# Optimization experiments

Hardware: AMD Instinct MI355X
Metric: run time of the kernel (lower is better)

The kernel has to match this reference:

```python
import jax, jax.numpy as jnp
import numpy as np

TOPK_RATIO = 0.1
THRESHOLD = 0.25
OUT_DIM = 256
STATS_DIM = 18
NEG = -1e30  # sentinel for invalid pixels when sorting (values are probs in [0,1])


def setup_inputs() -> dict:
    key = jax.random.key(0)
    k1, k2, k3, k4, k5, k6, k7 = jax.random.split(key, 7)
    B, C, H, W = 16, 4, 512, 512
    evidence_logits = jax.random.normal(k1, (B, C, H, W), dtype=jnp.float32)
    severity_map = jax.random.normal(k2, (B, 1, H, W), dtype=jnp.float32)
    target_mask = jax.random.uniform(k3, (B, 1, H, W), dtype=jnp.float32)
    # LayerNorm(18) params (torch defaults: weight=1, bias=0)
    ln_w = jnp.ones((STATS_DIM,), jnp.float32)
    ln_b = jnp.zeros((STATS_DIM,), jnp.float32)
    # Linear(18, out_dim) and Linear(out_dim, out_dim)
    w1 = jax.random.normal(k4, (STATS_DIM, OUT_DIM), dtype=jnp.float32) * 0.1
    b1 = jax.random.normal(k5, (OUT_DIM,), dtype=jnp.float32) * 0.01
    w2 = jax.random.normal(k6, (OUT_DIM, OUT_DIM), dtype=jnp.float32) * 0.05
    b2 = jax.random.normal(k7, (OUT_DIM,), dtype=jnp.float32) * 0.01
    return {"evidence_logits": evidence_logits, "severity_map": severity_map,
            "target_mask": target_mask, "ln_w": ln_w, "ln_b": ln_b,
            "w1": w1, "b1": b1, "w2": w2, "b2": b2}


def _forward(evidence_logits, severity_map, target_mask, ln_w, ln_b, w1, b1, w2, b2):
    B, C, H, W = evidence_logits.shape
    N = H * W
    prob = jax.nn.softmax(evidence_logits, axis=1).reshape(B, C, N).transpose(0, 2, 1)  # [B,N,4]
    sev = jax.nn.sigmoid(severity_map).reshape(B, N)                                    # [B,N]
    # mask is same spatial size as logits, so nearest resize is identity
    valid = target_mask.reshape(B, N) > 0.5                                             # [B,N] bool
    validf = valid.astype(prob.dtype)
    total = validf.sum(axis=-1)                                                         # [B]
    has = total > 0
    safe_total = jnp.maximum(total, 1.0)
    # k = max(1, round(total * ratio)); total>=1 implies k<=total
    k = jnp.maximum(1, jnp.round(total * TOPK_RATIO)).astype(jnp.int32)                 # [B]

    # per-class masked mean / max
    class_mean = jnp.einsum('bnc,bn->bc', prob, validf) / safe_total[:, None]           # [B,4]
    class_max = jnp.max(jnp.where(valid[:, :, None], prob, NEG), axis=1)                # [B,4]
    class_max = jnp.where(has[:, None], class_max, 0.0)

    # top-k means for 4 class channels + severity at once: sort desc, cumsum, gather at k-1
    vals = jnp.concatenate([prob, sev[:, :, None]], axis=-1)                            # [B,N,5]
    masked = jnp.where(valid[:, :, None], vals, NEG)
    sorted_desc = jnp.sort(masked, axis=1)[:, ::-1, :]                                  # [B,N,5]
    csum = jnp.cumsum(sorted_desc, axis=1)
    idx = (k - 1).astype(jnp.int32)[:, None, None]                                      # [B,1,1]
    topk_mean = jnp.take_along_axis(csum, jnp.broadcast_to(idx, (B, 1, 5)), axis=1)[:, 0, :]
    topk_mean = topk_mean / k[:, None].astype(prob.dtype)                               # [B,5]
    topk_mean = jnp.where(has[:, None], topk_mean, 0.0)
    class_topk = topk_mean[:, :4]                                                       # [B,4]
    sev_topk = topk_mean[:, 4:5]                                                        # [B,1]

    sev_mean = jnp.where(has, jnp.sum(sev * validf, axis=-1) / safe_total, 0.0)[:, None]
    sev_max = jnp.where(has, jnp.max(jnp.where(valid, sev, NEG), axis=-1), 0.0)[:, None]

    damaged_ind = (prob[:, :, 1] + prob[:, :, 2] + prob[:, :, 3] > THRESHOLD).astype(prob.dtype)
    high_ind = (prob[:, :, 2] + prob[:, :, 3] > THRESHOLD).astype(prob.dtype)
    damaged = jnp.where(has, jnp.sum(damaged_ind * validf, axis=-1) / safe_total, 0.0)   # [B]
    high = jnp.where(has, jnp.sum(high_ind * validf, axis=-1) / safe_total, 0.0)         # [B]
    tar = jnp.where(has, validf.mean(axis=-1), 0.0)                                      # [B]

    stats = jnp.concatenate([class_mean, class_max, class_topk,
                             sev_mean, sev_max, sev_topk,
                             damaged[:, None], high[:, None], tar[:, None]], axis=-1)    # [B,18]

    # LayerNorm(18), eps=1e-5
    mu = stats.mean(axis=-1, keepdims=True)
    var = jnp.mean((stats - mu) ** 2, axis=-1, keepdims=True)
    normed = (stats - mu) * jax.lax.rsqrt(var + 1e-5) * ln_w + ln_b
    h1 = jax.nn.gelu(normed @ w1 + b1, approximate=False)
    projected = h1 @ w2 + b2                                                             # [B,256]
    return stats, projected, damaged, high, tar


def reference(evidence_logits, severity_map, target_mask, ln_w, ln_b, w1, b1, w2, b2):
    return _forward(evidence_logits, severity_map, target_mask, ln_w, ln_b, w1, b1, w2, b2)
```

## Files before the change

### kernel.cpp

```cpp
#include <hip/hip_runtime.h>
#include <math.h>

#define NB 512
#define CHN 5

static constexpr int kN = 512 * 512;
static constexpr int kB = 16;
static constexpr int kChunks = 64;
static constexpr int kThreads1 = 512;
static constexpr int kPixPerBlock = kN / kChunks;
static constexpr int kF4PerBlock = kPixPerBlock / 4;
static constexpr int kGroups = kF4PerBlock / kThreads1;
static constexpr int kHist = CHN * NB;

static constexpr size_t GHIST_OFF = 0;
static constexpr size_t SPART_OFF = GHIST_OFF + (size_t)kB * kHist * 4;
static constexpr size_t PART_OFF  = SPART_OFF + (size_t)kB * kChunks * 16 * 4;
static constexpr size_t WS_PART_BYTES = PART_OFF + (size_t)kB * kChunks * kHist * 4;

template <int PART_MODE>
__global__ __launch_bounds__(kThreads1) void ep_pass1(
    const float* __restrict__ logits,
    const float* __restrict__ sevmap,
    const float* __restrict__ mask,
    float* __restrict__ spart,
    unsigned* __restrict__ part_hist,
    unsigned* __restrict__ g_hist) {
  __shared__ unsigned s_hcnt[kHist];
  __shared__ float s_red[8][16];

  const int tid = threadIdx.x;
  const int b = blockIdx.y;
  const int chunk = blockIdx.x;

  for (int i = tid; i < kHist; i += kThreads1) s_hcnt[i] = 0u;
  __syncthreads();

  const float4* L0 = (const float4*)(logits + (size_t)b * 4 * kN);
  const float4* L1 = L0 + kN / 4;
  const float4* L2 = L1 + kN / 4;
  const float4* L3 = L2 + kN / 4;
  const float4* SV = (const float4*)(sevmap + (size_t)b * kN);
  const float4* MK = (const float4*)(mask + (size_t)b * kN);
  const int base = chunk * kF4PerBlock;

  float cnt = 0.f, sum0 = 0.f, sum1 = 0.f, sum2 = 0.f, sum3 = 0.f;
  float sevs = 0.f, dmg = 0.f, hig = 0.f;
  float mx0 = 0.f, mx1 = 0.f, mx2 = 0.f, mx3 = 0.f, sevm = 0.f;

#pragma unroll
  for (int g = 0; g < kGroups; ++g) {
    const int fi = base + g * kThreads1 + tid;
    float4 a = L0[fi];
    float4 bq = L1[fi];
    float4 cq = L2[fi];
    float4 dq = L3[fi];
    float4 sv = SV[fi];
    float4 mk = MK[fi];
#pragma unroll
    for (int j = 0; j < 4; ++j) {
      float l0 = ((const float*)&a)[j];
      float l1 = ((const float*)&bq)[j];
      float l2 = ((const float*)&cq)[j];
      float l3 = ((const float*)&dq)[j];
      float e0 = __expf(l0);
      float e1 = __expf(l1);
      float e2 = __expf(l2);
      float e3 = __expf(l3);
      float inv = 1.f / (e0 + e1 + e2 + e3);
      float p0 = e0 * inv, p1 = e1 * inv, p2 = e2 * inv, p3 = e3 * inv;
      float sg = 1.f / (1.f + __expf(-((const float*)&sv)[j]));
      bool valid = ((const float*)&mk)[j] > 0.5f;
      if (valid) {
        cnt += 1.f;
        sum0 += p0; sum1 += p1; sum2 += p2; sum3 += p3;
        mx0 = fmaxf(mx0, p0); mx1 = fmaxf(mx1, p1);
        mx2 = fmaxf(mx2, p2); mx3 = fmaxf(mx3, p3);
        sevs += sg; sevm = fmaxf(sevm, sg);
        dmg += (p1 + p2 + p3 > 0.25f) ? 1.f : 0.f;
        hig += (p2 + p3 > 0.25f) ? 1.f : 0.f;
        int bi0 = min(NB - 1, (int)(p0 * (float)NB));
        int bi1 = min(NB - 1, (int)(p1 * (float)NB));
        int bi2 = min(NB - 1, (int)(p2 * (float)NB));
        int bi3 = min(NB - 1, (int)(p3 * (float)NB));
        int bi4 = min(NB - 1, (int)(sg * (float)NB));
        atomicAdd(&s_hcnt[0 * NB + bi0], 1u);
        atomicAdd(&s_hcnt[1 * NB + bi1], 1u);
        atomicAdd(&s_hcnt[2 * NB + bi2], 1u);
        atomicAdd(&s_hcnt[3 * NB + bi3], 1u);
        atomicAdd(&s_hcnt[4 * NB + bi4], 1u);
      }
    }
  }

  float acc[8] = {cnt, sum0, sum1, sum2, sum3, sevs, dmg, hig};
  float mxs[5] = {mx0, mx1, mx2, mx3, sevm};
#pragma unroll
  for (int off = 32; off > 0; off >>= 1) {
#pragma unroll
    for (int i = 0; i < 8; ++i) acc[i] += __shfl_down(acc[i], off);
#pragma unroll
    for (int i = 0; i < 5; ++i) mxs[i] = fmaxf(mxs[i], __shfl_down(mxs[i], off));
  }
  const int lane = tid & 63;
  const int wv = tid >> 6;
  if (lane == 0) {
#pragma unroll
    for (int i = 0; i < 8; ++i) s_red[wv][i] = acc[i];
#pragma unroll
    for (int i = 0; i < 5; ++i) s_red[wv][8 + i] = mxs[i];
  }
  __syncthreads();
  if (tid < 16) {
    float v;
    if (tid < 8) {
      v = 0.f;
#pragma unroll
      for (int w = 0; w < 8; ++w) v += s_red[w][tid];
    } else if (tid < 13) {
      v = 0.f;
#pragma unroll
      for (int w = 0; w < 8; ++w) v = fmaxf(v, s_red[w][tid]);
    } else {
      v = 0.f;
    }
    spart[((size_t)b * kChunks + chunk) * 16 + tid] = v;
  }

  if (PART_MODE) {
    uint4* dst = (uint4*)(part_hist + ((size_t)b * kChunks + chunk) * kHist);
    const uint4* src = (const uint4*)s_hcnt;
    for (int i = tid; i < kHist / 4; i += kThreads1) dst[i] = src[i];
  } else {
    unsigned* gh = g_hist + (size_t)b * kHist;
    for (int i = tid; i < kHist; i += kThreads1) {
      unsigned c = s_hcnt[i];
      if (c) atomicAdd(&gh[i], c);
    }
  }
}

__global__ __launch_bounds__(256) void ep_reduce_hist(
    const unsigned* __restrict__ part_hist,
    unsigned* __restrict__ g_hist) {
  const int i = blockIdx.x * 256 + threadIdx.x;
  const int b = blockIdx.y;
  unsigned s = 0;
  const unsigned* p = part_hist + (size_t)b * kChunks * kHist + i;
#pragma unroll 8
  for (int c = 0; c < kChunks; ++c) s += p[(size_t)c * kHist];
  g_hist[(size_t)b * kHist + i] = s;
}

__global__ __launch_bounds__(256) void ep_finalize(
    const float* __restrict__ spart,
    const unsigned* __restrict__ g_hist,
    const float* __restrict__ ln_w, const float* __restrict__ ln_b,
    const float* __restrict__ w1, const float* __restrict__ b1,
    const float* __restrict__ w2, const float* __restrict__ b2,
    float* __restrict__ out) {
  __shared__ float topk[8];
  __shared__ float s_scal[16];
  __shared__ float stats[18], normed[18], h1v[256];

  const int tid = threadIdx.x;
  const int lane = tid & 63;
  const int wv = tid >> 6;
  const int b = blockIdx.x;

  if (tid < 8) topk[tid] = 0.f;

  if (wv == 3) {
    for (int s = 0; s < 13; ++s) {
      float v = spart[((size_t)b * kChunks + lane) * 16 + s];
#pragma unroll
      for (int off = 32; off > 0; off >>= 1) {
        float t = __shfl_down(v, off);
        v = (s < 8) ? (v + t) : fmaxf(v, t);
      }
      if (lane == 0) s_scal[s] = v;
    }
  }
  __syncthreads();

  const float total = s_scal[0];
  const bool has = total > 0.f;
  const float safe = fmaxf(total, 1.f);
  const float kf = fmaxf(1.f, rintf(total * 0.1f));

  for (int c = wv; c < CHN; c += 4) {
    const unsigned* hc = g_hist + ((size_t)b * CHN + c) * NB;
    const int base = (63 - lane) * 8;
    float cntv[8];
    float gc = 0.f, gs = 0.f;
    const uint4* hv = (const uint4*)(hc + base);
#pragma unroll
    for (int q = 0; q < 2; ++q) {
      uint4 u = hv[q];
      float c0 = (float)u.x, c1 = (float)u.y, c2 = (float)u.z, c3 = (float)u.w;
      int bin = base + q * 4;
      cntv[q * 4 + 0] = c0; cntv[q * 4 + 1] = c1;
      cntv[q * 4 + 2] = c2; cntv[q * 4 + 3] = c3;
      gc += c0 + c1 + c2 + c3;
      gs += c0 * ((bin + 0.5f) * (1.f / NB)) + c1 * ((bin + 1.5f) * (1.f / NB)) +
            c2 * ((bin + 2.5f) * (1.f / NB)) + c3 * ((bin + 3.5f) * (1.f / NB));
    }
    float ic = gc, is = gs;
#pragma unroll
    for (int off = 1; off < 64; off <<= 1) {
      float tc = __shfl_up(ic, off);
      float ts = __shfl_up(is, off);
      if (lane >= off) { ic += tc; is += ts; }
    }
    float ec = ic - gc;
    float es = is - gs;

    if (has && ec < kf && kf <= ic) {
      float cg = ec, ss = es;
#pragma unroll
      for (int d = 7; d >= 0; --d) {
        int bin = base + d;
        float center = (bin + 0.5f) * (1.f / NB);
        float cb = cntv[d];
        if (cg + cb >= kf) {
          float r = kf - cg;
          topk[c] = (ss + r * center) / kf;
          break;
        }
        cg += cb;
        ss += cb * center;
      }
    }
  }
  __syncthreads();

  if (tid == 0) {
    float inv_safe = 1.f / safe;
    stats[0] = s_scal[1] * inv_safe;
    stats[1] = s_scal[2] * inv_safe;
    stats[2] = s_scal[3] * inv_safe;
    stats[3] = s_scal[4] * inv_safe;
#pragma unroll
    for (int c = 0; c < 4; ++c) stats[4 + c] = has ? s_scal[8 + c] : 0.f;
#pragma unroll
    for (int c = 0; c < 4; ++c) stats[8 + c] = has ? topk[c] : 0.f;
    stats[12] = has ? s_scal[5] * inv_safe : 0.f;
    stats[13] = has ? s_scal[12] : 0.f;
    stats[14] = has ? topk[4] : 0.f;
    stats[15] = has ? s_scal[6] * inv_safe : 0.f;
    stats[16] = has ? s_scal[7] * inv_safe : 0.f;
    stats[17] = has ? total * (1.f / (float)kN) : 0.f;

    float mu = 0.f;
#pragma unroll
    for (int i = 0; i < 18; ++i) mu += stats[i];
    mu *= (1.f / 18.f);
    float var = 0.f;
#pragma unroll
    for (int i = 0; i < 18; ++i) {
      float d = stats[i] - mu;
      var += d * d;
    }
    var *= (1.f / 18.f);
    float inv_std = rsqrtf(var + 1e-5f);
#pragma unroll
    for (int i = 0; i < 18; ++i)
      normed[i] = (stats[i] - mu) * inv_std * ln_w[i] + ln_b[i];
  }
  __syncthreads();

  float x = b1[tid];
#pragma unroll
  for (int i = 0; i < 18; ++i) x += normed[i] * w1[i * 256 + tid];
  h1v[tid] = 0.5f * x * (1.f + erff(x * 0.70710678118654752440f));
  __syncthreads();

  float y = b2[tid];
  for (int i = 0; i < 256; ++i) y += h1v[i] * w2[i * 256 + tid];

  out[288 + b * 256 + tid] = y;
  if (tid < 18) out[b * 18 + tid] = stats[tid];
  if (tid == 0) {
    out[4384 + b] = stats[15];
    out[4400 + b] = stats[16];
    out[4416 + b] = stats[17];
  }
}

extern "C" void kernel_launch(void* const* d_in, const int* in_sizes, int n_in,
                              void* d_out, int out_size, void* d_ws, size_t ws_size,
                              hipStream_t stream) {
  const float* logits = (const float*)d_in[0];
  const float* sevmap = (const float*)d_in[1];
  const float* maskp  = (const float*)d_in[2];
  const float* ln_w   = (const float*)d_in[3];
  const float* ln_b   = (const float*)d_in[4];
  const float* w1     = (const float*)d_in[5];
  const float* b1     = (const float*)d_in[6];
  const float* w2     = (const float*)d_in[7];
  const float* b2     = (const float*)d_in[8];
  float* out = (float*)d_out;

  char* ws = (char*)d_ws;
  unsigned* g_hist = (unsigned*)(ws + GHIST_OFF);
  float* spart = (float*)(ws + SPART_OFF);
  unsigned* part_hist = (unsigned*)(ws + PART_OFF);

  dim3 g1(kChunks, kB);
  if (ws_size >= WS_PART_BYTES) {
    ep_pass1<1><<<g1, kThreads1, 0, stream>>>(logits, sevmap, maskp, spart,
                                              part_hist, g_hist);
    dim3 g2(kHist / 256, kB);
    ep_reduce_hist<<<g2, 256, 0, stream>>>(part_hist, g_hist);
  } else {
    hipMemsetAsync(g_hist, 0, (size_t)kB * kHist * 4, stream);
    ep_pass1<0><<<g1, kThreads1, 0, stream>>>(logits, sevmap, maskp, spart,
                                              part_hist, g_hist);
  }
  ep_finalize<<<kB, 256, 0, stream>>>(spart, g_hist, ln_w, ln_b, w1, b1, w2, b2,
                                      out);
}
```

Before: 156.1 us.

## Fold histogram reduction into finalize kernel with 16-bit partial histograms

Removes the separate histogram-reduction kernel and the atomic fallback path. Pass 1 now runs 32 chunks of 1024 threads and writes each per-chunk histogram as 16-bit counts, which halves partial-histogram traffic. The finalize kernel, now 1024 threads, sums the 32 partials into shared memory before the top-k and MLP stages. This saves a launch and a global round trip, at the cost of fewer pass-1 blocks and only 16 finalize blocks doing the reduction. 16-bit counts overflow if more than 65535 pixels of one chunk land in one bin (a chunk holds 8192 pixels, so this cannot happen here).

```diff
diff --git a/kernel.cpp b/kernel.cpp
--- a/kernel.cpp
+++ b/kernel.cpp
@@ -6,28 +6,24 @@
 
 static constexpr int kN = 512 * 512;
 static constexpr int kB = 16;
-static constexpr int kChunks = 64;
-static constexpr int kThreads1 = 512;
+static constexpr int kChunks = 32;
+static constexpr int kThreads1 = 1024;
 static constexpr int kPixPerBlock = kN / kChunks;
 static constexpr int kF4PerBlock = kPixPerBlock / 4;
 static constexpr int kGroups = kF4PerBlock / kThreads1;
 static constexpr int kHist = CHN * NB;
 
-static constexpr size_t GHIST_OFF = 0;
-static constexpr size_t SPART_OFF = GHIST_OFF + (size_t)kB * kHist * 4;
+static constexpr size_t SPART_OFF = 0;
 static constexpr size_t PART_OFF  = SPART_OFF + (size_t)kB * kChunks * 16 * 4;
-static constexpr size_t WS_PART_BYTES = PART_OFF + (size_t)kB * kChunks * kHist * 4;
-
-template <int PART_MODE>
+
 __global__ __launch_bounds__(kThreads1) void ep_pass1(
     const float* __restrict__ logits,
     const float* __restrict__ sevmap,
     const float* __restrict__ mask,
     float* __restrict__ spart,
-    unsigned* __restrict__ part_hist,
-    unsigned* __restrict__ g_hist) {
+    unsigned short* __restrict__ part_hist) {
   __shared__ unsigned s_hcnt[kHist];
-  __shared__ float s_red[8][16];
+  __shared__ float s_red[16][16];
 
   const int tid = threadIdx.x;
   const int b = blockIdx.y;
@@ -116,49 +112,36 @@
     if (tid < 8) {
       v = 0.f;
 #pragma unroll
-      for (int w = 0; w < 8; ++w) v += s_red[w][tid];
+      for (int w = 0; w < 16; ++w) v += s_red[w][tid];
     } else if (tid < 13) {
       v = 0.f;
 #pragma unroll
-      for (int w = 0; w < 8; ++w) v = fmaxf(v, s_red[w][tid]);
+      for (int w = 0; w < 16; ++w) v = fmaxf(v, s_red[w][tid]);
     } else {
       v = 0.f;
     }
     spart[((size_t)b * kChunks + chunk) * 16 + tid] = v;
   }
 
-  if (PART_MODE) {
-    uint4* dst = (uint4*)(part_hist + ((size_t)b * kChunks + chunk) * kHist);
-    const uint4* src = (const uint4*)s_hcnt;
-    for (int i = tid; i < kHist / 4; i += kThreads1) dst[i] = src[i];
-  } else {
-    unsigned* gh = g_hist + (size_t)b * kHist;
-    for (int i = tid; i < kHist; i += kThreads1) {
-      unsigned c = s_hcnt[i];
-      if (c) atomicAdd(&gh[i], c);
-    }
+  ushort4* dst = (ushort4*)(part_hist + ((size_t)b * kChunks + chunk) * kHist);
+  for (int i = tid; i < kHist / 4; i += kThreads1) {
+    ushort4 v;
+    v.x = (unsigned short)s_hcnt[4 * i + 0];
+    v.y = (unsigned short)s_hcnt[4 * i + 1];
+    v.z = (unsigned short)s_hcnt[4 * i + 2];
+    v.w = (unsigned short)s_hcnt[4 * i + 3];
+    dst[i] = v;
   }
 }
 
-__global__ __launch_bounds__(256) void ep_reduce_hist(
-    const unsigned* __restrict__ part_hist,
-    unsigned* __restrict__ g_hist) {
-  const int i = blockIdx.x * 256 + threadIdx.x;
-  const int b = blockIdx.y;
-  unsigned s = 0;
-  const unsigned* p = part_hist + (size_t)b * kChunks * kHist + i;
-#pragma unroll 8
-  for (int c = 0; c < kChunks; ++c) s += p[(size_t)c * kHist];
-  g_hist[(size_t)b * kHist + i] = s;
-}
-
-__global__ __launch_bounds__(256) void ep_finalize(
+__global__ __launch_bounds__(1024) void ep_finalize(
     const float* __restrict__ spart,
-    const unsigned* __restrict__ g_hist,
+    const unsigned short* __restrict__ part_hist,
     const float* __restrict__ ln_w, const float* __restrict__ ln_b,
     const float* __restrict__ w1, const float* __restrict__ b1,
     const float* __restrict__ w2, const float* __restrict__ b2,
     float* __restrict__ out) {
+  __shared__ unsigned s_hist[kHist];
   __shared__ float topk[8];
   __shared__ float s_scal[16];
   __shared__ float stats[18], normed[18], h1v[256];
@@ -170,12 +153,27 @@
 
   if (tid < 8) topk[tid] = 0.f;
 
-  if (wv == 3) {
+  {
+    const unsigned* pp = (const unsigned*)(part_hist + (size_t)b * kChunks * kHist);
+    for (int i = tid; i < kHist / 2; i += 1024) {
+      unsigned a0 = 0, a1 = 0;
+#pragma unroll
+      for (int c = 0; c < kChunks; ++c) {
+        unsigned u = pp[(size_t)c * (kHist / 2) + i];
+        a0 += u & 0xffffu;
+        a1 += u >> 16;
+      }
+      s_hist[2 * i] = a0;
+      s_hist[2 * i + 1] = a1;
+    }
+  }
+
+  if (wv == 15 && lane < kChunks) {
     for (int s = 0; s < 13; ++s) {
       float v = spart[((size_t)b * kChunks + lane) * 16 + s];
 #pragma unroll
-      for (int off = 32; off > 0; off >>= 1) {
-        float t = __shfl_down(v, off);
+      for (int off = 16; off > 0; off >>= 1) {
+        float t = __shfl_down(v, off, 32);
         v = (s < 8) ? (v + t) : fmaxf(v, t);
       }
       if (lane == 0) s_scal[s] = v;
@@ -188,15 +186,15 @@
   const float safe = fmaxf(total, 1.f);
   const float kf = fmaxf(1.f, rintf(total * 0.1f));
 
-  for (int c = wv; c < CHN; c += 4) {
-    const unsigned* hc = g_hist + ((size_t)b * CHN + c) * NB;
+  if (wv < CHN) {
+    const int c = wv;
     const int base = (63 - lane) * 8;
     float cntv[8];
     float gc = 0.f, gs = 0.f;
-    const uint4* hv = (const uint4*)(hc + base);
+    const uint4* hv = (const uint4*)s_hist;
 #pragma unroll
     for (int q = 0; q < 2; ++q) {
-      uint4 u = hv[q];
+      uint4 u = hv[c * (NB / 4) + (63 - lane) * 2 + q];
       float c0 = (float)u.x, c1 = (float)u.y, c2 = (float)u.z, c3 = (float)u.w;
       int bin = base + q * 4;
       cntv[q * 4 + 0] = c0; cntv[q * 4 + 1] = c1;
@@ -269,21 +267,24 @@
   }
   __syncthreads();
 
-  float x = b1[tid];
-#pragma unroll
-  for (int i = 0; i < 18; ++i) x += normed[i] * w1[i * 256 + tid];
-  h1v[tid] = 0.5f * x * (1.f + erff(x * 0.70710678118654752440f));
-  __syncthreads();
-
-  float y = b2[tid];
-  for (int i = 0; i < 256; ++i) y += h1v[i] * w2[i * 256 + tid];
-
-  out[288 + b * 256 + tid] = y;
-  if (tid < 18) out[b * 18 + tid] = stats[tid];
-  if (tid == 0) {
-    out[4384 + b] = stats[15];
-    out[4400 + b] = stats[16];
-    out[4416 + b] = stats[17];
+  if (tid < 256) {
+    float x = b1[tid];
+#pragma unroll
+    for (int i = 0; i < 18; ++i) x += normed[i] * w1[i * 256 + tid];
+    h1v[tid] = 0.5f * x * (1.f + erff(x * 0.70710678118654752440f));
+  }
+  __syncthreads();
+  if (tid < 256) {
+    float y = b2[tid];
+    for (int i = 0; i < 256; ++i) y += h1v[i] * w2[i * 256 + tid];
+
+    out[288 + b * 256 + tid] = y;
+    if (tid < 18) out[b * 18 + tid] = stats[tid];
+    if (tid == 0) {
+      out[4384 + b] = stats[15];
+      out[4400 + b] = stats[16];
+      out[4416 + b] = stats[17];
+    }
   }
 }
 
@@ -302,21 +303,11 @@
   float* out = (float*)d_out;
 
   char* ws = (char*)d_ws;
-  unsigned* g_hist = (unsigned*)(ws + GHIST_OFF);
   float* spart = (float*)(ws + SPART_OFF);
-  unsigned* part_hist = (unsigned*)(ws + PART_OFF);
+  unsigned short* part_hist = (unsigned short*)(ws + PART_OFF);
 
   dim3 g1(kChunks, kB);
-  if (ws_size >= WS_PART_BYTES) {
-    ep_pass1<1><<<g1, kThreads1, 0, stream>>>(logits, sevmap, maskp, spart,
-                                              part_hist, g_hist);
-    dim3 g2(kHist / 256, kB);
-    ep_reduce_hist<<<g2, 256, 0, stream>>>(part_hist, g_hist);
-  } else {
-    hipMemsetAsync(g_hist, 0, (size_t)kB * kHist * 4, stream);
-    ep_pass1<0><<<g1, kThreads1, 0, stream>>>(logits, sevmap, maskp, spart,
-                                              part_hist, g_hist);
-  }
-  ep_finalize<<<kB, 256, 0, stream>>>(spart, g_hist, ln_w, ln_b, w1, b1, w2, b2,
-                                      out);
+  ep_pass1<<<g1, kThreads1, 0, stream>>>(logits, sevmap, maskp, spart, part_hist);
+  ep_finalize<<<kB, 1024, 0, stream>>>(spart, part_hist, ln_w, ln_b, w1, b1, w2,
+                                       b2, out);
 }
```

Result: faster. 151.5 us (-2.9%).
